# Performance work log

Hardware: AMD Instinct MI355X
Metric: run time of the kernel (lower is better)

The kernel has to match this reference:

```python
import jax, jax.numpy as jnp
import numpy as np

B, OBS, LAT, NXT, E, HG, H = 8192, 128, 32, 128, 8, 256, 256


def setup_inputs() -> dict:
    key = jax.random.key(0)
    ks = jax.random.split(key, 20)
    d_in = OBS + LAT

    def w(k, shape, fan_in):
        return jax.random.uniform(k, shape, jnp.float32, -1.0, 1.0) * (np.sqrt(3.0) / np.sqrt(fan_in)).astype(np.float32)

    inp = {
        "x": jax.random.normal(ks[0], (B, OBS), jnp.float32),
        "z": jax.random.normal(ks[1], (B, LAT), jnp.float32),
        # gating MLP: (obs+lat) -> hg -> hg -> hg -> E
        "gw0": w(ks[2], (d_in, HG), d_in), "gb0": jnp.zeros((HG,), jnp.float32),
        "gw1": w(ks[3], (HG, HG), HG),    "gb1": jnp.zeros((HG,), jnp.float32),
        "gw2": w(ks[4], (HG, HG), HG),    "gb2": jnp.zeros((HG,), jnp.float32),
        "gw3": w(ks[5], (HG, E), HG),     "gb3": jnp.zeros((E,), jnp.float32),
        # expert weight stacks (kaiming-uniform-style init, bias = 0.01)
        "w0": w(ks[6], (E, d_in, H), d_in * H),      "b0": jnp.full((E, H), 0.01, jnp.float32),
        "w1": w(ks[7], (E, H + LAT, H), (H + LAT) * H), "b1": jnp.full((E, H), 0.01, jnp.float32),
        "w2": w(ks[8], (E, H + LAT, NXT), (H + LAT) * NXT), "b2": jnp.full((E, NXT), 0.01, jnp.float32),
    }
    return inp


def reference(x, z, gw0, gb0, gw1, gb1, gw2, gb2, gw3, gb3, w0, b0, w1, b1, w2, b2):
    xz = jnp.concatenate((x, z), axis=1)  # [B, obs+lat]
    # gating MLP (ELU activations, linear head) -> softmax coefficients over experts
    g = jax.nn.elu(xz @ gw0 + gb0)
    g = jax.nn.elu(g @ gw1 + gb1)
    g = jax.nn.elu(g @ gw2 + gb2)
    coef = jax.nn.softmax(g @ gw3 + gb3, axis=1)  # [B, E]

    layer_out = x
    for w, b, act in ((w0, b0, jax.nn.elu), (w1, b1, jax.nn.elu), (w2, b2, None)):
        inp = jnp.concatenate((layer_out, z), axis=1)  # [B, i]
        # coefficient-weighted expert mixing fused with the per-sample matvec:
        # equals (coef @ flat_weight).view(B,i,o) consumed by baddbmm in the original
        out = jnp.einsum('bi,eio,be->bo', inp, w, coef) + coef @ b
        layer_out = act(out) if act is not None else out
    return layer_out
```

## Files before the change

### kernel.cpp

```cpp
#include <hip/hip_runtime.h>
#include <hip/hip_bf16.h>

typedef _Float16 half_t;
typedef __attribute__((ext_vector_type(8))) _Float16 half8;
typedef __attribute__((ext_vector_type(4))) _Float16 half4;
typedef __attribute__((ext_vector_type(4))) float float4v;
typedef __attribute__((ext_vector_type(2))) float float2v;

#define BSZ 8192
#define NT 1024
#define ACTSTR 280
#define XSTR 152
#define ZSTR 40

#define OFF_SX 0
#define OFF_SB0 (OFF_SX + 32 * XSTR)
#define OFF_SB1 (OFF_SB0 + 32 * ACTSTR)
#define OFF_SZ (OFF_SB1 + 32 * ACTSTR)
#define HALFS_TOTAL (OFF_SZ + 32 * ZSTR)
#define OFF_LOG_B (HALFS_TOTAL * 2)
#define OFF_CF_B (OFF_LOG_B + 1024)
#define SMEM_BYTES 131072

__device__ __forceinline__ float elu_fast(float v) {
    return v > 0.f ? v : (__expf(v) - 1.f);
}

template <int EXPP, int NPASS, int CH, int MT, bool ZLAST, int ACT, int DST>
__device__ __forceinline__ void layer_run(
    const half_t* sSrc, int sstr, const half_t* sZ,
    const half_t* __restrict__ W, int NS,
    const float* __restrict__ bias, int biasN, const float* sCf,
    half_t* sDst, float* __restrict__ gOut, int ldg,
    int row0, int strip, int mrow, int lane, int l15, int quad) {
    constexpr int TOT = NPASS * CH;
    static_assert(TOT >= 2, "pipeline prologue needs >= 2 bodies");
    const size_t estr = (size_t)NS * CH * 512;
    const int col = strip * 16 + l15;
    const half_t* aBase = sSrc + (mrow + l15) * sstr + quad * 8;
    const half_t* zBase = sZ + (mrow + l15) * ZSTR + quad * 8;

    const half_t* wp = W + (size_t)strip * CH * 512 + lane * 8;
    int c_i = 0;
    const float* bp = bias + col;
    int c_c = 0, h_c = 0;

    half8 B0[EXPP], B1[EXPP], B2[EXPP], A0[MT], A1[MT], A2[MT];
    float part[MT][4];
    float bv[EXPP];
    float4v acc[EXPP][MT];

    auto issue = [&](half8(&B)[EXPP], half8(&A)[MT]) {
#pragma unroll
        for (int e = 0; e < EXPP; ++e) B[e] = *(const half8*)&wp[(size_t)e * estr];
#pragma unroll
        for (int mt = 0; mt < MT; ++mt)
            A[mt] = (ZLAST && c_i == CH - 1)
                        ? *(const half8*)&zBase[mt * 16 * ZSTR]
                        : *(const half8*)&aBase[mt * 16 * sstr + c_i * 32];
        wp += 512;
        if (++c_i == CH) { c_i = 0; wp += (size_t)EXPP * estr - (size_t)CH * 512; }
    };

    auto body = [&](half8(&B)[EXPP], half8(&A)[MT]) {
        if (c_c == 0) {
#pragma unroll
            for (int e = 0; e < EXPP; ++e) bv[e] = bp[(size_t)e * biasN];
#pragma unroll
            for (int e = 0; e < EXPP; ++e)
#pragma unroll
                for (int mt = 0; mt < MT; ++mt) acc[e][mt] = (float4v){0.f, 0.f, 0.f, 0.f};
        }
#pragma unroll
        for (int e = 0; e < EXPP; ++e)
#pragma unroll
            for (int mt = 0; mt < MT; ++mt)
                acc[e][mt] = __builtin_amdgcn_mfma_f32_16x16x32_f16(A[mt], B[e], acc[e][mt], 0, 0, 0);
        if (c_c == CH - 1) {
#pragma unroll
            for (int mt = 0; mt < MT; ++mt)
#pragma unroll
                for (int r = 0; r < 4; ++r) {
                    const int rl = mrow + mt * 16 + quad * 4 + r;
                    float val;
                    if constexpr (EXPP * NPASS == 1) {
                        val = acc[0][mt][r] + bv[0];
                    } else {
                        const float2v cf = *(const float2v*)&sCf[rl * 8 + h_c * EXPP];
                        val = cf[0] * (acc[0][mt][r] + bv[0]);
                        val += cf[1] * (acc[1][mt][r] + bv[1]);
                    }
                    part[mt][r] = (h_c == 0) ? val : part[mt][r] + val;
                    if (h_c == NPASS - 1) {
                        float o = part[mt][r];
                        if (DST == 0) {
                            if (ACT) o = elu_fast(o);
                            sDst[rl * ACTSTR + col] = (half_t)o;
                        } else {
                            gOut[(size_t)(row0 + rl) * ldg + col] = o;
                        }
                    }
                }
            bp += (size_t)EXPP * biasN;
        }
        if (++c_c == CH) { c_c = 0; ++h_c; }
    };

    issue(B0, A0);
    issue(B1, A1);
    int it = 0;
#pragma unroll 1
    for (; it + 5 <= TOT; it += 3) {
        issue(B2, A2);  body(B0, A0);
        issue(B0, A0);  body(B1, A1);
        issue(B1, A1);  body(B2, A2);
    }
    {
        const int R = TOT - it;
        if (R == 2) {
            body(B0, A0); body(B1, A1);
        } else if (R == 3) {
            issue(B2, A2); body(B0, A0); body(B1, A1); body(B2, A2);
        } else {
            issue(B2, A2); body(B0, A0);
            issue(B0, A0); body(B1, A1); body(B2, A2); body(B0, A0);
        }
    }
}

__device__ __forceinline__ void layer_logits(
    const half_t* sSrc, const half_t* __restrict__ W,
    const float* __restrict__ bias, float* sLog, int wv, int lane, int l15, int quad) {
    if (wv != 0) return;
    float4v acc[2] = {(float4v){0.f, 0.f, 0.f, 0.f}, (float4v){0.f, 0.f, 0.f, 0.f}};
#pragma unroll
    for (int c = 0; c < 8; ++c) {
        half8 a0 = *(const half8*)&sSrc[l15 * ACTSTR + c * 32 + quad * 8];
        half8 a1 = *(const half8*)&sSrc[(16 + l15) * ACTSTR + c * 32 + quad * 8];
        half8 b = *(const half8*)&W[c * 512 + lane * 8];
        acc[0] = __builtin_amdgcn_mfma_f32_16x16x32_f16(a0, b, acc[0], 0, 0, 0);
        acc[1] = __builtin_amdgcn_mfma_f32_16x16x32_f16(a1, b, acc[1], 0, 0, 0);
    }
    if (l15 < 8) {
        const float bvv = bias[l15];
#pragma unroll
        for (int mt = 0; mt < 2; ++mt)
#pragma unroll
            for (int r = 0; r < 4; ++r)
                sLog[(mt * 16 + quad * 4 + r) * 8 + l15] = acc[mt][r] + bvv;
    }
}

__global__ __launch_bounds__(NT) void fused_mann(
    const float* __restrict__ x, const float* __restrict__ z,
    const half_t* __restrict__ Wg0, const half_t* __restrict__ Wg1,
    const half_t* __restrict__ Wg2, const half_t* __restrict__ Wg3,
    const float* __restrict__ gb0, const float* __restrict__ gb1,
    const float* __restrict__ gb2, const float* __restrict__ gb3,
    const half_t* __restrict__ W0, const half_t* __restrict__ W1,
    const half_t* __restrict__ W2, const float* __restrict__ b0,
    const float* __restrict__ b1, const float* __restrict__ b2,
    float* __restrict__ out) {
    extern __shared__ __align__(16) char dynsm[];
    half_t* sm = (half_t*)dynsm;
    half_t* sX = sm + OFF_SX;
    half_t* sB0 = sm + OFF_SB0;
    half_t* sB1 = sm + OFF_SB1;
    half_t* sZ = sm + OFF_SZ;
    float* sLog = (float*)(dynsm + OFF_LOG_B);
    float* sCf = (float*)(dynsm + OFF_CF_B);

    const int tid = threadIdx.x;
    const int row0 = blockIdx.x * 32;
    const int lane = tid & 63, wv = tid >> 6;
    const int l15 = lane & 15, quad = lane >> 4;

    for (int i = tid; i < 32 * 128; i += NT) {
        int r = i >> 7, c = i & 127;
        sX[r * XSTR + c] = (half_t)x[(size_t)(row0 + r) * 128 + c];
    }
    for (int i = tid; i < 32 * 32; i += NT) {
        int r = i >> 5, c = i & 31;
        sZ[r * ZSTR + c] = (half_t)z[(size_t)(row0 + r) * 32 + c];
    }
    __syncthreads();

    layer_run<1, 1, 5, 2, true, 1, 0>(sX, XSTR, sZ, Wg0, 16, gb0, 256, nullptr,
                                      sB0, nullptr, 0, row0, wv, 0, lane, l15, quad);
    __syncthreads();
    layer_run<1, 1, 8, 2, false, 1, 0>(sB0, ACTSTR, sZ, Wg1, 16, gb1, 256, nullptr,
                                       sB1, nullptr, 0, row0, wv, 0, lane, l15, quad);
    __syncthreads();
    layer_run<1, 1, 8, 2, false, 1, 0>(sB1, ACTSTR, sZ, Wg2, 16, gb2, 256, nullptr,
                                       sB0, nullptr, 0, row0, wv, 0, lane, l15, quad);
    __syncthreads();
    layer_logits(sB0, Wg3, gb3, sLog, wv, lane, l15, quad);
    __syncthreads();
    if (tid < 32) {
        float v[8], m = -1e30f;
#pragma unroll
        for (int e = 0; e < 8; ++e) { v[e] = sLog[tid * 8 + e]; m = fmaxf(m, v[e]); }
        float sum = 0.f;
#pragma unroll
        for (int e = 0; e < 8; ++e) { v[e] = __expf(v[e] - m); sum += v[e]; }
        float inv = 1.f / sum;
#pragma unroll
        for (int e = 0; e < 8; ++e) sCf[tid * 8 + e] = v[e] * inv;
    }
    __syncthreads();
    layer_run<2, 4, 5, 2, true, 1, 0>(sX, XSTR, sZ, W0, 16, b0, 256, sCf,
                                      sB1, nullptr, 0, row0, wv, 0, lane, l15, quad);
    __syncthreads();
    layer_run<2, 4, 9, 2, true, 1, 0>(sB1, ACTSTR, sZ, W1, 16, b1, 256, sCf,
                                      sB0, nullptr, 0, row0, wv, 0, lane, l15, quad);
    __syncthreads();
    layer_run<2, 4, 9, 1, true, 0, 2>(sB0, ACTSTR, sZ, W2, 8, b2, 128, sCf,
                                      nullptr, out, 128, row0, wv & 7, (wv >> 3) * 16,
                                      lane, l15, quad);
}

struct WDesc { const float* src; half_t* dst; int K, N, Npad, blk0; };
struct WPack { WDesc d[7]; };

__global__ __launch_bounds__(256) void conv_w_all(WPack pk) {
    __shared__ float t[32][33];
    const int bid = blockIdx.x;
    int di = 0;
#pragma unroll
    for (int i = 1; i < 7; ++i)
        if (bid >= pk.d[i].blk0) di = i;
    const WDesc d = pk.d[di];
    const int NS = d.Npad >> 4, CHN = d.K >> 5;
    const int ntiles = d.Npad / 32, ktiles = CHN;
    int local = bid - d.blk0;
    const int e = local / (ktiles * ntiles);
    local %= ktiles * ntiles;
    const int k0 = (local / ntiles) * 32, n0 = (local % ntiles) * 32;
    const int tr = threadIdx.x >> 3;
    const int tc = (threadIdx.x & 7) * 4;

    float4 v = {0.f, 0.f, 0.f, 0.f};
    if (n0 + tc < d.N)
        v = *(const float4*)&d.src[((size_t)e * d.K + k0 + tr) * d.N + n0 + tc];
    t[tr][tc] = v.x; t[tr][tc + 1] = v.y; t[tr][tc + 2] = v.z; t[tr][tc + 3] = v.w;
    __syncthreads();
    half4 h;
#pragma unroll
    for (int i = 0; i < 4; ++i) h[i] = (half_t)t[tc + i][tr];
    const int n = n0 + tr;
    const size_t blk = ((size_t)e * NS + (n >> 4)) * CHN + (k0 >> 5);
    const int off = ((tc >> 3) * 16 + (n & 15)) * 8 + (tc & 7);
    *(half4*)&d.dst[blk * 512 + off] = h;
}

extern "C" void kernel_launch(void* const* d_in, const int* in_sizes, int n_in,
                              void* d_out, int out_size, void* d_ws, size_t ws_size,
                              hipStream_t stream) {
    const float* x   = (const float*)d_in[0];
    const float* z   = (const float*)d_in[1];
    const float* gw0 = (const float*)d_in[2];
    const float* gb0 = (const float*)d_in[3];
    const float* gw1 = (const float*)d_in[4];
    const float* gb1 = (const float*)d_in[5];
    const float* gw2 = (const float*)d_in[6];
    const float* gb2 = (const float*)d_in[7];
    const float* gw3 = (const float*)d_in[8];
    const float* gb3 = (const float*)d_in[9];
    const float* w0  = (const float*)d_in[10];
    const float* b0  = (const float*)d_in[11];
    const float* w1  = (const float*)d_in[12];
    const float* b1  = (const float*)d_in[13];
    const float* w2  = (const float*)d_in[14];
    const float* b2  = (const float*)d_in[15];

    char* p = (char*)d_ws;
    auto take = [&](size_t bytes) { char* r = p; p += bytes; return r; };
    half_t* Wg0 = (half_t*)take((size_t)256 * 160 * 2);
    half_t* Wg1 = (half_t*)take((size_t)256 * 256 * 2);
    half_t* Wg2 = (half_t*)take((size_t)256 * 256 * 2);
    half_t* Wg3 = (half_t*)take((size_t)32 * 256 * 2);
    half_t* W0  = (half_t*)take((size_t)8 * 256 * 160 * 2);
    half_t* W1  = (half_t*)take((size_t)8 * 256 * 288 * 2);
    half_t* W2  = (half_t*)take((size_t)8 * 128 * 288 * 2);
    float* out  = (float*)d_out;

    WPack pk;
    int blk = 0;
    auto mk = [&](int i, const float* s, half_t* dst, int K, int N, int Npad, int E) {
        pk.d[i] = WDesc{s, dst, K, N, Npad, blk};
        blk += E * (K / 32) * (Npad / 32);
    };
    mk(0, gw0, Wg0, 160, 256, 256, 1);
    mk(1, gw1, Wg1, 256, 256, 256, 1);
    mk(2, gw2, Wg2, 256, 256, 256, 1);
    mk(3, gw3, Wg3, 256, 8, 32, 1);
    mk(4, w0, W0, 160, 256, 256, 8);
    mk(5, w1, W1, 288, 256, 256, 8);
    mk(6, w2, W2, 288, 128, 128, 8);

    hipFuncSetAttribute((const void*)fused_mann,
                        hipFuncAttributeMaxDynamicSharedMemorySize, SMEM_BYTES);

    conv_w_all<<<dim3(blk), dim3(256), 0, stream>>>(pk);
    fused_mann<<<dim3(BSZ / 32), dim3(NT), SMEM_BYTES, stream>>>(
        x, z, Wg0, Wg1, Wg2, Wg3, gb0, gb1, gb2, gb3,
        W0, W1, W2, b0, b1, b2, out);
}
```

Before: 130.7 us.

## Halve rows per block and split final layer experts across waves with smem reduction

Each block now processes 16 rows instead of 32, doubling the grid to 512 blocks so the 256-CU device gets more blocks and shared memory per block shrinks. The last layer no longer gives each wave group 16 rows. Instead, the two wave halves each take half of the expert passes and write partial sums to a shared reduction buffer, and a final pass adds them and stores to global memory. The trade-off is that every block must re-read the full weight set, so weight traffic per row doubles. It also adds a barrier and a reduction step.

```diff
diff --git a/kernel.cpp b/kernel.cpp
--- a/kernel.cpp
+++ b/kernel.cpp
@@ -8,19 +8,21 @@
 typedef __attribute__((ext_vector_type(2))) float float2v;
 
 #define BSZ 8192
+#define ROWS 16
 #define NT 1024
 #define ACTSTR 280
 #define XSTR 152
 #define ZSTR 40
 
 #define OFF_SX 0
-#define OFF_SB0 (OFF_SX + 32 * XSTR)
-#define OFF_SB1 (OFF_SB0 + 32 * ACTSTR)
-#define OFF_SZ (OFF_SB1 + 32 * ACTSTR)
-#define HALFS_TOTAL (OFF_SZ + 32 * ZSTR)
+#define OFF_SB0 (OFF_SX + ROWS * XSTR)
+#define OFF_SB1 (OFF_SB0 + ROWS * ACTSTR)
+#define OFF_SZ (OFF_SB1 + ROWS * ACTSTR)
+#define HALFS_TOTAL (OFF_SZ + ROWS * ZSTR)
 #define OFF_LOG_B (HALFS_TOTAL * 2)
-#define OFF_CF_B (OFF_LOG_B + 1024)
-#define SMEM_BYTES 131072
+#define OFF_CF_B (OFF_LOG_B + 512)
+#define OFF_RED_B (OFF_CF_B + 512)
+#define SMEM_BYTES (OFF_RED_B + 16384)
 
 __device__ __forceinline__ float elu_fast(float v) {
     return v > 0.f ? v : (__expf(v) - 1.f);
@@ -31,8 +33,8 @@
     const half_t* sSrc, int sstr, const half_t* sZ,
     const half_t* __restrict__ W, int NS,
     const float* __restrict__ bias, int biasN, const float* sCf,
-    half_t* sDst, float* __restrict__ gOut, int ldg,
-    int row0, int strip, int mrow, int lane, int l15, int quad) {
+    half_t* sDst, float* gOut, int ldg,
+    int row0, int strip, int mrow, int hbase, int lane, int l15, int quad) {
     constexpr int TOT = NPASS * CH;
     static_assert(TOT >= 2, "pipeline prologue needs >= 2 bodies");
     const size_t estr = (size_t)NS * CH * 512;
@@ -40,9 +42,9 @@
     const half_t* aBase = sSrc + (mrow + l15) * sstr + quad * 8;
     const half_t* zBase = sZ + (mrow + l15) * ZSTR + quad * 8;
 
-    const half_t* wp = W + (size_t)strip * CH * 512 + lane * 8;
+    const half_t* wp = W + (size_t)strip * CH * 512 + lane * 8 + (size_t)hbase * EXPP * estr;
     int c_i = 0;
-    const float* bp = bias + col;
+    const float* bp = bias + col + (size_t)hbase * EXPP * biasN;
     int c_c = 0, h_c = 0;
 
     half8 B0[EXPP], B1[EXPP], B2[EXPP], A0[MT], A1[MT], A2[MT];
@@ -83,21 +85,27 @@
                 for (int r = 0; r < 4; ++r) {
                     const int rl = mrow + mt * 16 + quad * 4 + r;
                     float val;
-                    if constexpr (EXPP * NPASS == 1) {
+                    if constexpr (EXPP * NPASS == 1 && DST == 0) {
+                        val = acc[0][mt][r] + bv[0];
+                        if (false) (void)val;
+                    }
+                    if constexpr (EXPP == 1) {
                         val = acc[0][mt][r] + bv[0];
                     } else {
-                        const float2v cf = *(const float2v*)&sCf[rl * 8 + h_c * EXPP];
+                        const float2v cf = *(const float2v*)&sCf[rl * 8 + (hbase + h_c) * EXPP];
                         val = cf[0] * (acc[0][mt][r] + bv[0]);
                         val += cf[1] * (acc[1][mt][r] + bv[1]);
                     }
                     part[mt][r] = (h_c == 0) ? val : part[mt][r] + val;
                     if (h_c == NPASS - 1) {
                         float o = part[mt][r];
-                        if (DST == 0) {
+                        if constexpr (DST == 0) {
                             if (ACT) o = elu_fast(o);
                             sDst[rl * ACTSTR + col] = (half_t)o;
+                        } else if constexpr (DST == 2) {
+                            gOut[(size_t)(row0 + rl) * ldg + col] = o;
                         } else {
-                            gOut[(size_t)(row0 + rl) * ldg + col] = o;
+                            gOut[rl * 16 + l15] = o;
                         }
                     }
                 }
@@ -132,22 +140,18 @@
     const half_t* sSrc, const half_t* __restrict__ W,
     const float* __restrict__ bias, float* sLog, int wv, int lane, int l15, int quad) {
     if (wv != 0) return;
-    float4v acc[2] = {(float4v){0.f, 0.f, 0.f, 0.f}, (float4v){0.f, 0.f, 0.f, 0.f}};
+    float4v acc = (float4v){0.f, 0.f, 0.f, 0.f};
 #pragma unroll
     for (int c = 0; c < 8; ++c) {
-        half8 a0 = *(const half8*)&sSrc[l15 * ACTSTR + c * 32 + quad * 8];
-        half8 a1 = *(const half8*)&sSrc[(16 + l15) * ACTSTR + c * 32 + quad * 8];
+        half8 a = *(const half8*)&sSrc[l15 * ACTSTR + c * 32 + quad * 8];
         half8 b = *(const half8*)&W[c * 512 + lane * 8];
-        acc[0] = __builtin_amdgcn_mfma_f32_16x16x32_f16(a0, b, acc[0], 0, 0, 0);
-        acc[1] = __builtin_amdgcn_mfma_f32_16x16x32_f16(a1, b, acc[1], 0, 0, 0);
+        acc = __builtin_amdgcn_mfma_f32_16x16x32_f16(a, b, acc, 0, 0, 0);
     }
     if (l15 < 8) {
         const float bvv = bias[l15];
 #pragma unroll
-        for (int mt = 0; mt < 2; ++mt)
-#pragma unroll
-            for (int r = 0; r < 4; ++r)
-                sLog[(mt * 16 + quad * 4 + r) * 8 + l15] = acc[mt][r] + bvv;
+        for (int r = 0; r < 4; ++r)
+            sLog[(quad * 4 + r) * 8 + l15] = acc[r] + bvv;
     }
 }
 
@@ -169,34 +173,35 @@
     half_t* sZ = sm + OFF_SZ;
     float* sLog = (float*)(dynsm + OFF_LOG_B);
     float* sCf = (float*)(dynsm + OFF_CF_B);
+    float* sRed = (float*)(dynsm + OFF_RED_B);
 
     const int tid = threadIdx.x;
-    const int row0 = blockIdx.x * 32;
+    const int row0 = blockIdx.x * ROWS;
     const int lane = tid & 63, wv = tid >> 6;
     const int l15 = lane & 15, quad = lane >> 4;
 
-    for (int i = tid; i < 32 * 128; i += NT) {
+    for (int i = tid; i < ROWS * 128; i += NT) {
         int r = i >> 7, c = i & 127;
         sX[r * XSTR + c] = (half_t)x[(size_t)(row0 + r) * 128 + c];
     }
-    for (int i = tid; i < 32 * 32; i += NT) {
+    for (int i = tid; i < ROWS * 32; i += NT) {
         int r = i >> 5, c = i & 31;
         sZ[r * ZSTR + c] = (half_t)z[(size_t)(row0 + r) * 32 + c];
     }
     __syncthreads();
 
-    layer_run<1, 1, 5, 2, true, 1, 0>(sX, XSTR, sZ, Wg0, 16, gb0, 256, nullptr,
-                                      sB0, nullptr, 0, row0, wv, 0, lane, l15, quad);
-    __syncthreads();
-    layer_run<1, 1, 8, 2, false, 1, 0>(sB0, ACTSTR, sZ, Wg1, 16, gb1, 256, nullptr,
-                                       sB1, nullptr, 0, row0, wv, 0, lane, l15, quad);
-    __syncthreads();
-    layer_run<1, 1, 8, 2, false, 1, 0>(sB1, ACTSTR, sZ, Wg2, 16, gb2, 256, nullptr,
-                                       sB0, nullptr, 0, row0, wv, 0, lane, l15, quad);
+    layer_run<1, 1, 5, 1, true, 1, 0>(sX, XSTR, sZ, Wg0, 16, gb0, 256, nullptr,
+                                      sB0, nullptr, 0, row0, wv, 0, 0, lane, l15, quad);
+    __syncthreads();
+    layer_run<1, 1, 8, 1, false, 1, 0>(sB0, ACTSTR, sZ, Wg1, 16, gb1, 256, nullptr,
+                                       sB1, nullptr, 0, row0, wv, 0, 0, lane, l15, quad);
+    __syncthreads();
+    layer_run<1, 1, 8, 1, false, 1, 0>(sB1, ACTSTR, sZ, Wg2, 16, gb2, 256, nullptr,
+                                       sB0, nullptr, 0, row0, wv, 0, 0, lane, l15, quad);
     __syncthreads();
     layer_logits(sB0, Wg3, gb3, sLog, wv, lane, l15, quad);
     __syncthreads();
-    if (tid < 32) {
+    if (tid < ROWS) {
         float v[8], m = -1e30f;
 #pragma unroll
         for (int e = 0; e < 8; ++e) { v[e] = sLog[tid * 8 + e]; m = fmaxf(m, v[e]); }
@@ -208,15 +213,23 @@
         for (int e = 0; e < 8; ++e) sCf[tid * 8 + e] = v[e] * inv;
     }
     __syncthreads();
-    layer_run<2, 4, 5, 2, true, 1, 0>(sX, XSTR, sZ, W0, 16, b0, 256, sCf,
-                                      sB1, nullptr, 0, row0, wv, 0, lane, l15, quad);
-    __syncthreads();
-    layer_run<2, 4, 9, 2, true, 1, 0>(sB1, ACTSTR, sZ, W1, 16, b1, 256, sCf,
-                                      sB0, nullptr, 0, row0, wv, 0, lane, l15, quad);
-    __syncthreads();
-    layer_run<2, 4, 9, 1, true, 0, 2>(sB0, ACTSTR, sZ, W2, 8, b2, 128, sCf,
-                                      nullptr, out, 128, row0, wv & 7, (wv >> 3) * 16,
-                                      lane, l15, quad);
+    layer_run<2, 4, 5, 1, true, 1, 0>(sX, XSTR, sZ, W0, 16, b0, 256, sCf,
+                                      sB1, nullptr, 0, row0, wv, 0, 0, lane, l15, quad);
+    __syncthreads();
+    layer_run<2, 4, 9, 1, true, 1, 0>(sB1, ACTSTR, sZ, W1, 16, b1, 256, sCf,
+                                      sB0, nullptr, 0, row0, wv, 0, 0, lane, l15, quad);
+    __syncthreads();
+    layer_run<2, 2, 9, 1, true, 0, 3>(sB0, ACTSTR, sZ, W2, 8, b2, 128, sCf,
+                                      nullptr, sRed + wv * 256, 0, row0, wv & 7, 0,
+                                      (wv >> 3) * 2, lane, l15, quad);
+    __syncthreads();
+    for (int i = tid; i < ROWS * 128; i += NT) {
+        const int r = i >> 7, c = i & 127;
+        const int strip = c >> 4, cl = c & 15;
+        const float v = sRed[strip * 256 + r * 16 + cl] +
+                        sRed[(strip + 8) * 256 + r * 16 + cl];
+        out[(size_t)(row0 + r) * 128 + c] = v;
+    }
 }
 
 struct WDesc { const float* src; half_t* dst; int K, N, Npad, blk0; };
@@ -302,7 +315,7 @@
                         hipFuncAttributeMaxDynamicSharedMemorySize, SMEM_BYTES);
 
     conv_w_all<<<dim3(blk), dim3(256), 0, stream>>>(pk);
-    fused_mann<<<dim3(BSZ / 32), dim3(NT), SMEM_BYTES, stream>>>(
+    fused_mann<<<dim3(BSZ / ROWS), dim3(NT), SMEM_BYTES, stream>>>(
         x, z, Wg0, Wg1, Wg2, Wg3, gb0, gb1, gb2, gb3,
         W0, W1, W2, b0, b1, b2, out);
 }
```

After: 150.3 us. +14.9%, slower.
